# Kernel tuning notes

Hardware: AMD Instinct MI355X
Metric: run time of the kernel (lower is better)

Reference implementation:

```python
import jax, jax.numpy as jnp
import numpy as np

N_NODES = 100000
N_EDGES = 3200000


def _gcn_conv(x, src, dst, norm_e, W, b, n_nodes):
    # PyG GCNConv: x @ W, propagate with symmetric norm (self-loops already
    # appended to src/dst with their norm coefficients in norm_e), then + b.
    h = x @ W                                    # [N, out]
    msgs = h[src] * norm_e[:, None]              # [E+N, out] gather + scale
    out = jax.ops.segment_sum(msgs, dst, num_segments=n_nodes)
    return out + b


def _prep_graph(edge_index, n_nodes):
    # Add self-loops and compute symmetric GCN normalization coefficients.
    src, dst = edge_index[0], edge_index[1]
    loops = jnp.arange(n_nodes, dtype=src.dtype)
    src = jnp.concatenate([src, loops])
    dst = jnp.concatenate([dst, loops])
    deg = jax.ops.segment_sum(jnp.ones_like(dst, dtype=jnp.float32), dst,
                              num_segments=n_nodes)
    dinv = jnp.where(deg > 0, jax.lax.rsqrt(deg), 0.0)
    norm_e = dinv[src] * dinv[dst]               # [E+N]
    return src, dst, norm_e


def setup_inputs() -> dict:
    key = jax.random.key(0)
    ks = jax.random.split(key, 5)
    k = 11  # max_colors + 1
    X = jax.random.normal(ks[0], (N_NODES, k), dtype=jnp.float32)
    edge_index = jax.random.randint(ks[1], (2, N_EDGES), 0, N_NODES,
                                    dtype=jnp.int64)
    # Glorot-ish scale for the tiny weight matrices.
    W1 = jax.random.normal(ks[2], (k, k), dtype=jnp.float32) * (1.0 / np.sqrt(k))
    W2 = jax.random.normal(ks[3], (k, k), dtype=jnp.float32) * (1.0 / np.sqrt(k))
    W3 = jax.random.normal(ks[4], (k, 10), dtype=jnp.float32) * (1.0 / np.sqrt(k))
    return {
        "X": X, "edge_index": edge_index,
        "W1": W1, "b1": jnp.zeros((k,), jnp.float32),
        "W2": W2, "b2": jnp.zeros((k,), jnp.float32),
        "W3": W3, "b3": jnp.zeros((10,), jnp.float32),
    }


def reference(X, edge_index, W1, b1, W2, b2, W3, b3):
    n_nodes = X.shape[0]
    src, dst, norm_e = _prep_graph(edge_index, n_nodes)
    h = _gcn_conv(X, src, dst, norm_e, W1, b1, n_nodes)
    h = jax.nn.gelu(h)
    h = _gcn_conv(h, src, dst, norm_e, W2, b2, n_nodes)
    h = jax.nn.gelu(h)
    h = _gcn_conv(h, src, dst, norm_e, W3, b3, n_nodes)
    return jax.nn.log_softmax(h, axis=1)
```

## Files before the change

kernel.cpp:

```cpp
#include <hip/hip_runtime.h>
#include <hip/hip_fp16.h>
#include <math.h>

#define N_NODES 100000
#define N_EDGES 3200000

#define NPBC  512
#define NBC   196
#define KB2   256
#define CH2   12500

#define HS    12

__device__ __forceinline__ float gelu_tanh(float x) {
    const float c = 0.7978845608028654f;
    float t = tanhf(c * (x + 0.044715f * x * x * x));
    return 0.5f * x * (1.0f + t);
}

__device__ __forceinline__ int detect_flag(const void* ei, int t, int* sflag) {
    if (t < 64) {
        unsigned int v = ((const unsigned int*)ei)[2 * t + 1];
        unsigned long long m = __ballot(v != 0u);
        if (t == 0) *sflag = (m != 0ull) ? 1 : 0;
    }
    __syncthreads();
    return *sflag;
}

__device__ __forceinline__ int load_idx(const void* ei, int f, size_t pos) {
    if (f) return ((const int*)ei)[pos];
    return (int)((const long long*)ei)[pos];
}

__global__ void cnt_kernel(const void* __restrict__ ei, int* __restrict__ bcnt) {
    __shared__ int lcnt[NBC];
    __shared__ int sflag;
    int k = blockIdx.x, t = threadIdx.x;
    int f = detect_flag(ei, t, &sflag);
    for (int b = t; b < NBC; b += 256) lcnt[b] = 0;
    __syncthreads();
    int lo = k * CH2, hi = min(lo + CH2, N_EDGES);
    for (int e = lo + t; e < hi; e += 256) {
        int d = load_idx(ei, f, (size_t)N_EDGES + e);
        atomicAdd(&lcnt[d >> 9], 1);
    }
    __syncthreads();
    for (int b = t; b < NBC; b += 256) bcnt[(size_t)k * NBC + b] = lcnt[b];
}

__global__ void prefix_kernel(int* __restrict__ bcnt, int* __restrict__ tot,
                              int* __restrict__ bbase, int* __restrict__ off) {
    __shared__ int sh[256];
    int t = threadIdx.x;
    int run = 0;
    if (t < NBC) {
#pragma unroll 4
        for (int k = 0; k < KB2; k++) {
            int v = bcnt[(size_t)k * NBC + t];
            bcnt[(size_t)k * NBC + t] = run;
            run += v;
        }
    }
    sh[t] = (t < NBC) ? run : 0;
    __syncthreads();
    int val = sh[t];
    for (int o = 1; o < 256; o <<= 1) {
        int add = (t >= o) ? sh[t - o] : 0;
        __syncthreads();
        val += add;
        sh[t] = val;
        __syncthreads();
    }
    if (t < NBC) {
        tot[t] = run;
        bbase[t] = val - run;
    }
    if (t == 0) off[N_NODES] = N_EDGES;
}

__global__ void part2_kernel(const void* __restrict__ ei, const int* __restrict__ boff,
                             const int* __restrict__ bbase, int* __restrict__ btmp) {
    __shared__ int lcnt[NBC];
    __shared__ int lbase[NBC];
    __shared__ int sflag;
    int k = blockIdx.x, t = threadIdx.x;
    int f = detect_flag(ei, t, &sflag);
    for (int b = t; b < NBC; b += 256) {
        lcnt[b] = 0;
        lbase[b] = bbase[b] + boff[(size_t)k * NBC + b];
    }
    __syncthreads();
    int lo = k * CH2, hi = min(lo + CH2, N_EDGES);
    for (int e = lo + t; e < hi; e += 256) {
        int s = load_idx(ei, f, e);
        int d = load_idx(ei, f, (size_t)N_EDGES + e);
        int b = d >> 9;
        int pos = atomicAdd(&lcnt[b], 1);
        btmp[lbase[b] + pos] = s | ((d & (NPBC - 1)) << 17);
    }
}

__global__ void build2_kernel(const int* __restrict__ tot, const int* __restrict__ bbase,
                              const int* __restrict__ btmp, int* __restrict__ csr,
                              int* __restrict__ off, float* __restrict__ dinv,
                              const float* __restrict__ X, const float* __restrict__ W,
                              __half* __restrict__ h2) {
    __shared__ int lcnt[NPBC];
    __shared__ int lcur[NPBC];
    __shared__ int ssc[NPBC];
    int b = blockIdx.x;
    int t = threadIdx.x;
    int cnt = tot[b];
    int base = bbase[b];
    lcnt[t] = 0;
    __syncthreads();
    const int* bt = btmp + base;
    for (int i = t; i < cnt; i += NPBC) atomicAdd(&lcnt[bt[i] >> 17], 1);
    __syncthreads();
    int c = lcnt[t];
    ssc[t] = c;
    __syncthreads();
    int val = c;
    for (int o = 1; o < NPBC; o <<= 1) {
        int add = (t >= o) ? ssc[t - o] : 0;
        __syncthreads();
        val += add;
        ssc[t] = val;
        __syncthreads();
    }
    int excl = val - c;
    lcur[t] = excl;
    int node = b * NPBC + t;
    float di = rsqrtf((float)c + 1.0f);
    if (node < N_NODES) {
        off[node] = base + excl;
        dinv[node] = di;
    }
    __syncthreads();
    for (int i = t; i < cnt; i += NPBC) {
        int e = bt[i];
        int p = atomicAdd(&lcur[e >> 17], 1);
        csr[base + p] = e & 0x1FFFF;
    }
    if (node < N_NODES) {
        float x[11];
#pragma unroll
        for (int i = 0; i < 11; i++) x[i] = X[(size_t)node * 11 + i];
#pragma unroll
        for (int j = 0; j < 11; j++) {
            float a = 0.0f;
#pragma unroll
            for (int i = 0; i < 11; i++) a += x[i] * W[i * 11 + j];
            h2[(size_t)node * HS + j] = __float2half(di * a);
        }
        h2[(size_t)node * HS + 11] = __float2half(0.0f);
    }
}

__device__ __forceinline__ void acc_row(const __half* __restrict__ h2, int n, float* a) {
    const __half* r = h2 + (size_t)n * HS;
    uint4 u = *(const uint4*)r;
    uint2 v = *(const uint2*)(r + 8);
    union { unsigned int u; __half2 h; } cv;
    float2 f;
    cv.u = u.x; f = __half22float2(cv.h); a[0] += f.x; a[1] += f.y;
    cv.u = u.y; f = __half22float2(cv.h); a[2] += f.x; a[3] += f.y;
    cv.u = u.z; f = __half22float2(cv.h); a[4] += f.x; a[5] += f.y;
    cv.u = u.w; f = __half22float2(cv.h); a[6] += f.x; a[7] += f.y;
    cv.u = v.x; f = __half22float2(cv.h); a[8] += f.x; a[9] += f.y;
    cv.u = v.y; f = __half22float2(cv.h); a[10] += f.x;
}

__device__ __forceinline__ void gather8(const int* __restrict__ csr, int lo, int hi, int p,
                                        const __half* __restrict__ h2in, float* a) {
    int e = lo + p;
    if (e >= hi) return;
    int s = csr[e];
    for (e += 8; e < hi; e += 8) {
        int s_next = csr[e];
        acc_row(h2in, s, a);
        s = s_next;
    }
    acc_row(h2in, s, a);
}

template <int OUT>
__global__ void mid_kernel(const int* __restrict__ off, const int* __restrict__ csr,
                           const __half* __restrict__ h2in, const float* __restrict__ bias,
                           const float* __restrict__ W, const float* __restrict__ dinv,
                           __half* __restrict__ h2out) {
    int tid = blockIdx.x * blockDim.x + threadIdx.x;
    int n = tid >> 3;
    int p = tid & 7;
    if (n >= N_NODES) return;
    int lo = off[n], hi = off[n + 1];
    float a[11];
#pragma unroll
    for (int i = 0; i < 11; i++) a[i] = 0.0f;
    if (p == 0) acc_row(h2in, n, a);
    gather8(csr, lo, hi, p, h2in, a);
#pragma unroll
    for (int i = 0; i < 11; i++) {
        a[i] += __shfl_xor(a[i], 1);
        a[i] += __shfl_xor(a[i], 2);
        a[i] += __shfl_xor(a[i], 4);
    }
    float di = dinv[n];
    float t[11];
#pragma unroll
    for (int i = 0; i < 11; i++) t[i] = gelu_tanh(di * a[i] + bias[i]);
#pragma unroll
    for (int j0 = 0; j0 < 2; j0++) {
        int j = p + 8 * j0;
        if (j >= HS) continue;
        float o = 0.0f;
        if (j < OUT) {
            float acc = 0.0f;
#pragma unroll
            for (int i = 0; i < 11; i++) acc += t[i] * W[i * OUT + j];
            o = di * acc;
        }
        h2out[(size_t)n * HS + j] = __float2half(o);
    }
}

__global__ void final_kernel(const int* __restrict__ off, const int* __restrict__ csr,
                             const __half* __restrict__ h2in, const float* __restrict__ bias,
                             const float* __restrict__ dinv, float* __restrict__ out) {
    int tid = blockIdx.x * blockDim.x + threadIdx.x;
    int n = tid >> 3;
    int p = tid & 7;
    if (n >= N_NODES) return;
    int lo = off[n], hi = off[n + 1];
    float a[11];
#pragma unroll
    for (int i = 0; i < 11; i++) a[i] = 0.0f;
    if (p == 0) acc_row(h2in, n, a);
    gather8(csr, lo, hi, p, h2in, a);
#pragma unroll
    for (int i = 0; i < 10; i++) {
        a[i] += __shfl_xor(a[i], 1);
        a[i] += __shfl_xor(a[i], 2);
        a[i] += __shfl_xor(a[i], 4);
    }
    float di = dinv[n];
    float t[10];
    float m = -1e30f;
#pragma unroll
    for (int j = 0; j < 10; j++) {
        t[j] = di * a[j] + bias[j];
        m = fmaxf(m, t[j]);
    }
    float s = 0.0f;
#pragma unroll
    for (int j = 0; j < 10; j++) s += expf(t[j] - m);
    float ls = logf(s);
    for (int j = p; j < 10; j += 8) out[(size_t)n * 10 + j] = t[j] - m - ls;
}

extern "C" void kernel_launch(void* const* d_in, const int* in_sizes, int n_in,
                              void* d_out, int out_size, void* d_ws, size_t ws_size,
                              hipStream_t stream) {
    const float* X  = (const float*)d_in[0];
    const void*  ei = d_in[1];
    const float* W1 = (const float*)d_in[2];
    const float* b1 = (const float*)d_in[3];
    const float* W2 = (const float*)d_in[4];
    const float* b2 = (const float*)d_in[5];
    const float* W3 = (const float*)d_in[6];
    const float* b3 = (const float*)d_in[7];
    float* out = (float*)d_out;

    const size_t N = N_NODES;
    const size_t E = N_EDGES;
    __half* h2a = (__half*)d_ws;
    __half* h2b = h2a + (size_t)HS * N;
    int*   csr  = (int*)(h2b + (size_t)HS * N);
    int*   btmp = csr + E;
    int*   bcnt = btmp + E;
    int*   tot  = bcnt + (size_t)KB2 * NBC;
    int*   bbase= tot + NBC + 4;
    int*   off  = bbase + NBC + 4;
    float* dinv = (float*)(off + N + 4);

    const int gb8 = (8 * N_NODES + 255) / 256;

    cnt_kernel<<<KB2, 256, 0, stream>>>(ei, bcnt);
    prefix_kernel<<<1, 256, 0, stream>>>(bcnt, tot, bbase, off);
    part2_kernel<<<KB2, 256, 0, stream>>>(ei, bcnt, bbase, btmp);
    build2_kernel<<<NBC, NPBC, 0, stream>>>(tot, bbase, btmp, csr, off, dinv,
                                            X, W1, h2a);
    mid_kernel<11><<<gb8, 256, 0, stream>>>(off, csr, h2a, b1, W2, dinv, h2b);
    mid_kernel<10><<<gb8, 256, 0, stream>>>(off, csr, h2b, b2, W3, dinv, h2a);
    final_kernel<<<gb8, 256, 0, stream>>>(off, csr, h2a, b3, dinv, out);
}
```

Before: 171.3 us.

## Parallelize bucket prefix across wavefronts and widen per-node gather to 16 lanes

The single-block serial column prefix over 256 chunk counts is replaced by a multi-block kernel in which one wavefront scans each bucket's column with shuffles, followed by a small scan over the bucket totals. Separately, the three aggregation kernels now assign 16 lanes per node instead of 8. Each lane therefore handles about two edges of the roughly 33 per node, which raises memory-level parallelism for the random row gathers. The cost is one extra kernel launch, one extra shuffle stage, and twice as many threads. Those threads also do the redundant gelu/softmax epilogue.

Measured after the change: 157.4 us (median of 3 runs). 1.09x faster.

```diff
diff --git a/kernel.cpp b/kernel.cpp
--- a/kernel.cpp
+++ b/kernel.cpp
@@ -49,22 +49,41 @@
     for (int b = t; b < NBC; b += 256) bcnt[(size_t)k * NBC + b] = lcnt[b];
 }
 
-__global__ void prefix_kernel(int* __restrict__ bcnt, int* __restrict__ tot,
-                              int* __restrict__ bbase, int* __restrict__ off) {
+__global__ void bprefix_kernel(int* __restrict__ bcnt, int* __restrict__ tot) {
+    int gid = blockIdx.x * blockDim.x + threadIdx.x;
+    int w = gid >> 6;
+    int l = gid & 63;
+    if (w >= NBC) return;
+    int v[4];
+    int s = 0;
+#pragma unroll
+    for (int i = 0; i < 4; i++) {
+        v[i] = bcnt[(size_t)(l * 4 + i) * NBC + w];
+        s += v[i];
+    }
+    int scan = s;
+#pragma unroll
+    for (int o = 1; o < 64; o <<= 1) {
+        int x = __shfl_up(scan, o);
+        if (l >= o) scan += x;
+    }
+    int run = scan - s;
+#pragma unroll
+    for (int i = 0; i < 4; i++) {
+        bcnt[(size_t)(l * 4 + i) * NBC + w] = run;
+        run += v[i];
+    }
+    if (l == 63) tot[w] = scan;
+}
+
+__global__ void bscan_kernel(const int* __restrict__ tot, int* __restrict__ bbase,
+                             int* __restrict__ off) {
     __shared__ int sh[256];
     int t = threadIdx.x;
-    int run = 0;
-    if (t < NBC) {
-#pragma unroll 4
-        for (int k = 0; k < KB2; k++) {
-            int v = bcnt[(size_t)k * NBC + t];
-            bcnt[(size_t)k * NBC + t] = run;
-            run += v;
-        }
-    }
-    sh[t] = (t < NBC) ? run : 0;
-    __syncthreads();
-    int val = sh[t];
+    int v = (t < NBC) ? tot[t] : 0;
+    sh[t] = v;
+    __syncthreads();
+    int val = v;
     for (int o = 1; o < 256; o <<= 1) {
         int add = (t >= o) ? sh[t - o] : 0;
         __syncthreads();
@@ -72,11 +91,8 @@
         sh[t] = val;
         __syncthreads();
     }
-    if (t < NBC) {
-        tot[t] = run;
-        bbase[t] = val - run;
-    }
-    if (t == 0) off[N_NODES] = N_EDGES;
+    if (t < NBC) bbase[t] = val - v;
+    if (t == NBC - 1) off[N_NODES] = val;
 }
 
 __global__ void part2_kernel(const void* __restrict__ ei, const int* __restrict__ boff,
@@ -172,12 +188,12 @@
     cv.u = v.y; f = __half22float2(cv.h); a[10] += f.x;
 }
 
-__device__ __forceinline__ void gather8(const int* __restrict__ csr, int lo, int hi, int p,
-                                        const __half* __restrict__ h2in, float* a) {
+__device__ __forceinline__ void gather16(const int* __restrict__ csr, int lo, int hi, int p,
+                                         const __half* __restrict__ h2in, float* a) {
     int e = lo + p;
     if (e >= hi) return;
     int s = csr[e];
-    for (e += 8; e < hi; e += 8) {
+    for (e += 16; e < hi; e += 16) {
         int s_next = csr[e];
         acc_row(h2in, s, a);
         s = s_next;
@@ -191,37 +207,35 @@
                            const float* __restrict__ W, const float* __restrict__ dinv,
                            __half* __restrict__ h2out) {
     int tid = blockIdx.x * blockDim.x + threadIdx.x;
-    int n = tid >> 3;
-    int p = tid & 7;
+    int n = tid >> 4;
+    int p = tid & 15;
     if (n >= N_NODES) return;
     int lo = off[n], hi = off[n + 1];
     float a[11];
 #pragma unroll
     for (int i = 0; i < 11; i++) a[i] = 0.0f;
     if (p == 0) acc_row(h2in, n, a);
-    gather8(csr, lo, hi, p, h2in, a);
+    gather16(csr, lo, hi, p, h2in, a);
 #pragma unroll
     for (int i = 0; i < 11; i++) {
         a[i] += __shfl_xor(a[i], 1);
         a[i] += __shfl_xor(a[i], 2);
         a[i] += __shfl_xor(a[i], 4);
+        a[i] += __shfl_xor(a[i], 8);
     }
     float di = dinv[n];
     float t[11];
 #pragma unroll
     for (int i = 0; i < 11; i++) t[i] = gelu_tanh(di * a[i] + bias[i]);
-#pragma unroll
-    for (int j0 = 0; j0 < 2; j0++) {
-        int j = p + 8 * j0;
-        if (j >= HS) continue;
+    if (p < HS) {
         float o = 0.0f;
-        if (j < OUT) {
+        if (p < OUT) {
             float acc = 0.0f;
 #pragma unroll
-            for (int i = 0; i < 11; i++) acc += t[i] * W[i * OUT + j];
+            for (int i = 0; i < 11; i++) acc += t[i] * W[i * OUT + p];
             o = di * acc;
         }
-        h2out[(size_t)n * HS + j] = __float2half(o);
+        h2out[(size_t)n * HS + p] = __float2half(o);
     }
 }
 
@@ -229,20 +243,21 @@
                              const __half* __restrict__ h2in, const float* __restrict__ bias,
                              const float* __restrict__ dinv, float* __restrict__ out) {
     int tid = blockIdx.x * blockDim.x + threadIdx.x;
-    int n = tid >> 3;
-    int p = tid & 7;
+    int n = tid >> 4;
+    int p = tid & 15;
     if (n >= N_NODES) return;
     int lo = off[n], hi = off[n + 1];
     float a[11];
 #pragma unroll
     for (int i = 0; i < 11; i++) a[i] = 0.0f;
     if (p == 0) acc_row(h2in, n, a);
-    gather8(csr, lo, hi, p, h2in, a);
+    gather16(csr, lo, hi, p, h2in, a);
 #pragma unroll
     for (int i = 0; i < 10; i++) {
         a[i] += __shfl_xor(a[i], 1);
         a[i] += __shfl_xor(a[i], 2);
         a[i] += __shfl_xor(a[i], 4);
+        a[i] += __shfl_xor(a[i], 8);
     }
     float di = dinv[n];
     float t[10];
@@ -256,7 +271,7 @@
 #pragma unroll
     for (int j = 0; j < 10; j++) s += expf(t[j] - m);
     float ls = logf(s);
-    for (int j = p; j < 10; j += 8) out[(size_t)n * 10 + j] = t[j] - m - ls;
+    if (p < 10) out[(size_t)n * 10 + p] = t[p] - m - ls;
 }
 
 extern "C" void kernel_launch(void* const* d_in, const int* in_sizes, int n_in,
@@ -284,14 +299,16 @@
     int*   off  = bbase + NBC + 4;
     float* dinv = (float*)(off + N + 4);
 
-    const int gb8 = (8 * N_NODES + 255) / 256;
+    const int gb16 = (16 * N_NODES + 255) / 256;
+    const int pb = (NBC * 64 + 255) / 256;
 
     cnt_kernel<<<KB2, 256, 0, stream>>>(ei, bcnt);
-    prefix_kernel<<<1, 256, 0, stream>>>(bcnt, tot, bbase, off);
+    bprefix_kernel<<<pb, 256, 0, stream>>>(bcnt, tot);
+    bscan_kernel<<<1, 256, 0, stream>>>(tot, bbase, off);
     part2_kernel<<<KB2, 256, 0, stream>>>(ei, bcnt, bbase, btmp);
     build2_kernel<<<NBC, NPBC, 0, stream>>>(tot, bbase, btmp, csr, off, dinv,
                                             X, W1, h2a);
-    mid_kernel<11><<<gb8, 256, 0, stream>>>(off, csr, h2a, b1, W2, dinv, h2b);
-    mid_kernel<10><<<gb8, 256, 0, stream>>>(off, csr, h2b, b2, W3, dinv, h2a);
-    final_kernel<<<gb8, 256, 0, stream>>>(off, csr, h2a, b3, dinv, out);
-}
+    mid_kernel<11><<<gb16, 256, 0, stream>>>(off, csr, h2a, b1, W2, dinv, h2b);
+    mid_kernel<10><<<gb16, 256, 0, stream>>>(off, csr, h2b, b2, W3, dinv, h2a);
+    final_kernel<<<gb16, 256, 0, stream>>>(off, csr, h2a, b3, dinv, out);
+}
```
